# Optimization experiments

Hardware: AMD Instinct MI355X
Metric: run time of the kernel (lower is better)

## Reference

```python
import jax, jax.numpy as jnp
import numpy as np

QMIN, QMAX = -128.0, 127.0  # 8-bit signed activation range


def fq_act(x, s):
    """Fake-quantize activations: clip(round(x/s))*s with straight-through estimator."""
    y = jnp.clip(jnp.round(x / s), QMIN, QMAX) * s
    return x + jax.lax.stop_gradient(y - x)


def fq_weight(w):
    """Per-tensor max-abs symmetric (narrow-range) 8-bit weight fake-quant with STE."""
    s = jnp.max(jnp.abs(w)) / 127.0
    y = jnp.clip(jnp.round(w / s), -127.0, 127.0) * s
    return w + jax.lax.stop_gradient(y - w)


def conv1x1(x, w, b):
    # x: [b,c,h,w], w: [o,c] -> [b,o,h,w]
    return jnp.einsum('bchw,oc->bohw', x, w) + b[None, :, None, None]


def setup_inputs() -> dict:
    key = jax.random.key(0)
    ks = jax.random.split(key, 6)
    B, C, HC, H, W = 8, 64, 32, 64, 64
    x = jax.random.normal(ks[0], (B, C, H, W), dtype=jnp.float32)
    wq = jax.random.normal(ks[1], (HC, C), dtype=jnp.float32) * 0.05
    wk = jax.random.normal(ks[2], (HC, C), dtype=jnp.float32) * 0.05
    wv = jax.random.normal(ks[3], (HC, C), dtype=jnp.float32) * 0.05
    wp = jax.random.normal(ks[4], (C, HC), dtype=jnp.float32) * 0.05
    return {
        'x': x,
        'wq': wq, 'bq': jnp.zeros((HC,), jnp.float32),
        'wk': wk, 'bk': jnp.zeros((HC,), jnp.float32),
        'wv': wv, 'bv': jnp.zeros((HC,), jnp.float32),
        'wp': wp, 'bp': jnp.zeros((C,), jnp.float32),
        's_in': jnp.ones((1,), jnp.float32) * 0.0625,
        's_out': jnp.ones((1,), jnp.float32) * 0.0625,
    }


def reference(x, wq, bq, wk, bk, wv, bv, wp, bp, s_in, s_out):
    b, c, h, w = x.shape
    hc = wq.shape[0]
    n = h * w
    xq = fq_act(x, s_in)                              # quant_inp(x)
    q = conv1x1(xq, fq_weight(wq), bq).reshape(b, hc, n).transpose(0, 2, 1)  # [b,n,hc]
    k = conv1x1(xq, fq_weight(wk), bk).reshape(b, hc, n)                     # [b,hc,n]
    v = conv1x1(xq, fq_weight(wv), bv).reshape(b, hc, n).transpose(0, 2, 1)  # [b,n,hc]
    z = jax.nn.softmax(jnp.einsum('bqc,bck->bqk', q, k), axis=-1)            # [b,n,n]
    z = jnp.einsum('bqk,bkc->bqc', z, v).transpose(0, 2, 1).reshape(b, hc, h, w)
    z = fq_act(z, s_in)                               # quant_inp(z) (shared module/scale)
    out = xq + conv1x1(z, fq_weight(wp), bp)
    return fq_act(out, s_out)                         # self.act QuantIdentity
```

## Files before the change

### kernel.cpp

```cpp
#include <hip/hip_runtime.h>
#include <hip/hip_bf16.h>
#include <cstdint>
#include <cstddef>

#define NB 8
#define NC 64
#define NHC 32
#define NN 4096
#define LOG2E 1.44269504088896340736f

typedef short v8s __attribute__((ext_vector_type(8)));
typedef float v4f __attribute__((ext_vector_type(4)));
typedef unsigned int v4u __attribute__((ext_vector_type(4)));

__device__ __forceinline__ unsigned short f2b(float f) {
    unsigned int u = __builtin_bit_cast(unsigned int, f);
    u += 0x7fffu + ((u >> 16) & 1u);
    return (unsigned short)(u >> 16);
}
__device__ __forceinline__ float b2f(unsigned short s) {
    unsigned int u = ((unsigned int)s) << 16;
    return __builtin_bit_cast(float, u);
}
__device__ __forceinline__ unsigned int pack2_bf16(float a, float b) {
    unsigned int ua = __builtin_bit_cast(unsigned int, a);
    ua += 0x7fffu + ((ua >> 16) & 1u);
    unsigned int ub = __builtin_bit_cast(unsigned int, b);
    ub += 0x7fffu + ((ub >> 16) & 1u);
    return (ua >> 16) | (ub & 0xffff0000u);
}
__device__ __forceinline__ unsigned int trunc2_bf16(float a, float b) {
    return __builtin_amdgcn_perm(__builtin_bit_cast(unsigned int, b),
                                 __builtin_bit_cast(unsigned int, a), 0x07060302u);
}
__device__ __forceinline__ float wave_max(float v) {
    #pragma unroll
    for (int off = 1; off < 64; off <<= 1) v = fmaxf(v, __shfl_xor(v, off));
    return v;
}

__global__ __launch_bounds__(256) void k_qkv(
    const float* __restrict__ x,
    const float* __restrict__ wq, const float* __restrict__ wk, const float* __restrict__ wv,
    const float* __restrict__ bq, const float* __restrict__ bk, const float* __restrict__ bv,
    const float* __restrict__ s_in,
    unsigned short* __restrict__ xqb, unsigned short* __restrict__ qb,
    unsigned short* __restrict__ kb, unsigned short* __restrict__ vb)
{
    int blk = blockIdx.x;
    int b   = blk & 7;
    int seg = blk >> 3;
    int p0  = seg * 64;
    int tid = threadIdx.x;
    int wave = tid >> 6;
    int lane = tid & 63;

    __shared__ __align__(16) unsigned short xt[64][72];
    __shared__ __align__(16) unsigned short wlds[6144];
    __shared__ float red[3][4];

    float4 q0 = *(const float4*)(wq + tid * 8), q1 = *(const float4*)(wq + tid * 8 + 4);
    float4 k0 = *(const float4*)(wk + tid * 8), k1 = *(const float4*)(wk + tid * 8 + 4);
    float4 v0 = *(const float4*)(wv + tid * 8), v1 = *(const float4*)(wv + tid * 8 + 4);
    float mq = fmaxf(fmaxf(fmaxf(fabsf(q0.x), fabsf(q0.y)), fmaxf(fabsf(q0.z), fabsf(q0.w))),
                     fmaxf(fmaxf(fabsf(q1.x), fabsf(q1.y)), fmaxf(fabsf(q1.z), fabsf(q1.w))));
    float mk = fmaxf(fmaxf(fmaxf(fabsf(k0.x), fabsf(k0.y)), fmaxf(fabsf(k0.z), fabsf(k0.w))),
                     fmaxf(fmaxf(fabsf(k1.x), fabsf(k1.y)), fmaxf(fabsf(k1.z), fabsf(k1.w))));
    float mv = fmaxf(fmaxf(fmaxf(fabsf(v0.x), fabsf(v0.y)), fmaxf(fabsf(v0.z), fabsf(v0.w))),
                     fmaxf(fmaxf(fabsf(v1.x), fabsf(v1.y)), fmaxf(fabsf(v1.z), fabsf(v1.w))));
    mq = wave_max(mq); mk = wave_max(mk); mv = wave_max(mv);
    if (lane == 0) { red[0][wave] = mq; red[1][wave] = mk; red[2][wave] = mv; }
    __syncthreads();
    float sq = fmaxf(fmaxf(red[0][0], red[0][1]), fmaxf(red[0][2], red[0][3])) / 127.0f;
    float sk = fmaxf(fmaxf(red[1][0], red[1][1]), fmaxf(red[1][2], red[1][3])) / 127.0f;
    float sw = fmaxf(fmaxf(red[2][0], red[2][1]), fmaxf(red[2][2], red[2][3])) / 127.0f;
    {
        float eq[8] = {q0.x, q0.y, q0.z, q0.w, q1.x, q1.y, q1.z, q1.w};
        float ek[8] = {k0.x, k0.y, k0.z, k0.w, k1.x, k1.y, k1.z, k1.w};
        float ev[8] = {v0.x, v0.y, v0.z, v0.w, v1.x, v1.y, v1.z, v1.w};
        #pragma unroll
        for (int j = 0; j < 8; ++j) {
            wlds[0 * 2048 + tid * 8 + j] = f2b(fminf(fmaxf(rintf(eq[j] / sq), -127.f), 127.f) * sq);
            wlds[1 * 2048 + tid * 8 + j] = f2b(fminf(fmaxf(rintf(ek[j] / sk), -127.f), 127.f) * sk);
            wlds[2 * 2048 + tid * 8 + j] = f2b(fminf(fmaxf(rintf(ev[j] / sw), -127.f), 127.f) * sw);
        }
    }

    float sv = s_in[0];
    float sinv = 1.0f / sv;
    int jj = tid & 15;
    int c0 = tid >> 4;
    #pragma unroll
    for (int it = 0; it < 4; ++it) {
        int c = c0 + it * 16;
        size_t gi = ((size_t)(b * NC + c) << 12) + p0 + jj * 4;
        float4 xv = *(const float4*)(x + gi);
        float r0 = fminf(fmaxf(rintf(xv.x * sinv), -128.f), 127.f) * sv;
        float r1 = fminf(fmaxf(rintf(xv.y * sinv), -128.f), 127.f) * sv;
        float r2 = fminf(fmaxf(rintf(xv.z * sinv), -128.f), 127.f) * sv;
        float r3 = fminf(fmaxf(rintf(xv.w * sinv), -128.f), 127.f) * sv;
        *(uint2*)(xqb + gi) = make_uint2(pack2_bf16(r0, r1), pack2_bf16(r2, r3));
        xt[jj * 4 + 0][c] = f2b(r0);
        xt[jj * 4 + 1][c] = f2b(r1);
        xt[jj * 4 + 2][c] = f2b(r2);
        xt[jj * 4 + 3][c] = f2b(r3);
    }
    __syncthreads();

    int quad = lane >> 4;
    int l15  = lane & 15;

    v8s bf0 = *(const v8s*)(&xt[wave * 16 + l15][0  + quad * 8]);
    v8s bf1 = *(const v8s*)(&xt[wave * 16 + l15][32 + quad * 8]);

    int pos = p0 + wave * 16 + l15;
    size_t posg = (size_t)b * NN + pos;
    int g_v  = wave >> 1;
    int hi_v = wave & 1;
    int qs   = l15 >> 2;
    int rr   = l15 & 3;
    int jv   = hi_v * 4 + rr;
    size_t fb = (size_t)b * NN * NHC + (size_t)seg * 2048;
    const v4f zc = {0.f, 0.f, 0.f, 0.f};

    #pragma unroll
    for (int rb = 0; rb < 6; ++rb) {
        v8s a0 = *(const v8s*)(wlds + (rb * 16 + l15) * 64 + 0  + quad * 8);
        v8s a1 = *(const v8s*)(wlds + (rb * 16 + l15) * 64 + 32 + quad * 8);
        v4f t   = __builtin_amdgcn_mfma_f32_16x16x32_bf16(a0, bf0, zc, 0, 0, 0);
        v4f acc = __builtin_amdgcn_mfma_f32_16x16x32_bf16(a1, bf1, t, 0, 0, 0);

        int R0 = rb * 16 + quad * 4;
        float vals[4];
        #pragma unroll
        for (int r = 0; r < 4; ++r) {
            int R = R0 + r;
            float bias = (R < 32) ? bq[R] : (R < 64) ? bk[R - 32] : bv[R - 64];
            float vv = acc[r] + bias;
            if (R < 32) vv *= LOG2E;
            vals[r] = vv;
        }
        if (R0 < 32) {
            *(unsigned int*)(qb + posg * NHC + R0)     = pack2_bf16(vals[0], vals[1]);
            *(unsigned int*)(qb + posg * NHC + R0 + 2) = pack2_bf16(vals[2], vals[3]);
        } else if (R0 < 64) {
            int chb = R0 - 32;
            size_t sidx = fb + (size_t)wave * 512 + ((chb >> 3) * 16 + l15) * 8 + (chb & 7);
            *(uint2*)(kb + sidx) = make_uint2(pack2_bf16(vals[0], vals[1]),
                                              pack2_bf16(vals[2], vals[3]));
        } else {
            int h = rb - 4;
            #pragma unroll
            for (int r = 0; r < 4; ++r) {
                int lp = quad * 4 + r;
                size_t sidx = fb + (size_t)(2 * h + g_v) * 512 + (qs * 16 + lp) * 8 + jv;
                vb[sidx] = f2b(vals[r]);
            }
        }
    }
}

__global__ __launch_bounds__(256, 2) void k_attn(
    const unsigned short* __restrict__ qb, const unsigned short* __restrict__ kb,
    const unsigned short* __restrict__ vb, const unsigned short* __restrict__ xqb,
    const float* __restrict__ wp, const float* __restrict__ bp,
    const float* __restrict__ s_in, const float* __restrict__ s_out,
    float* __restrict__ out)
{
    int blk  = blockIdx.x;
    int b    = blk & 7;
    int qt   = blk >> 3;
    int qbase = qt * 64;
    int tid  = threadIdx.x;
    int wave = tid >> 6;
    int lane = tid & 63;
    int quad = lane >> 4;
    int l15  = lane & 15;

    __shared__ __align__(16) float zbuf[4][64][36];
    __shared__ float lbuf[4][64];
    __shared__ __align__(16) unsigned short wpq[2048];
    __shared__ float redw[4];

    {
        float4 a0 = *(const float4*)(wp + tid * 8), a1 = *(const float4*)(wp + tid * 8 + 4);
        float mx = fmaxf(fmaxf(fmaxf(fabsf(a0.x), fabsf(a0.y)), fmaxf(fabsf(a0.z), fabsf(a0.w))),
                         fmaxf(fmaxf(fabsf(a1.x), fabsf(a1.y)), fmaxf(fabsf(a1.z), fabsf(a1.w))));
        mx = wave_max(mx);
        if (lane == 0) redw[wave] = mx;
        __syncthreads();
        float scale = fmaxf(fmaxf(redw[0], redw[1]), fmaxf(redw[2], redw[3])) / 127.0f;
        float e[8] = {a0.x, a0.y, a0.z, a0.w, a1.x, a1.y, a1.z, a1.w};
        #pragma unroll
        for (int j = 0; j < 8; ++j) {
            float r = fminf(fmaxf(rintf(e[j] / scale), -127.f), 127.f);
            wpq[tid * 8 + j] = f2b(r * scale);
        }
    }

    const unsigned short* qbat = qb + (size_t)b * NN * NHC;
    const unsigned short* kft  = kb + (size_t)b * NN * NHC;
    const unsigned short* vft  = vb + (size_t)b * NN * NHC;

    v8s qf[4];
    #pragma unroll
    for (int s = 0; s < 4; ++s)
        qf[s] = *(const v8s*)(qbat + (qbase + s * 16 + l15) * NHC + quad * 8);

    const v4f zc = {0.f, 0.f, 0.f, 0.f};
    v4f zt[4][2] = {{zc, zc}, {zc, zc}, {zc, zc}, {zc, zc}};
    float psA[4] = {0.f, 0.f, 0.f, 0.f};
    float psB[4] = {0.f, 0.f, 0.f, 0.f};

    int lane8 = lane * 8;
    int t0 = wave * 16;

    const unsigned short* kp = kft + (size_t)t0 * 2048;
    const unsigned short* vp = vft + (size_t)t0 * 2048;
    v8s ck0 = *(const v8s*)(kp + 0 * 512 + lane8);
    v8s ck1 = *(const v8s*)(kp + 1 * 512 + lane8);
    v8s ck2 = *(const v8s*)(kp + 2 * 512 + lane8);
    v8s ck3 = *(const v8s*)(kp + 3 * 512 + lane8);
    v8s cv00 = *(const v8s*)(vp + 0 * 512 + lane8);
    v8s cv01 = *(const v8s*)(vp + 1 * 512 + lane8);
    v8s cv10 = *(const v8s*)(vp + 2 * 512 + lane8);
    v8s cv11 = *(const v8s*)(vp + 3 * 512 + lane8);

    #pragma unroll 1
    for (int i = 0; i < 16; ++i) {
        int ni = wave * 16 + ((i + 1) & 15);
        const unsigned short* kn = kft + (size_t)ni * 2048;
        const unsigned short* vn = vft + (size_t)ni * 2048;
        v8s nk0 = *(const v8s*)(kn + 0 * 512 + lane8);
        v8s nk1 = *(const v8s*)(kn + 1 * 512 + lane8);
        v8s nk2 = *(const v8s*)(kn + 2 * 512 + lane8);
        v8s nk3 = *(const v8s*)(kn + 3 * 512 + lane8);
        v8s nv00 = *(const v8s*)(vn + 0 * 512 + lane8);
        v8s nv01 = *(const v8s*)(vn + 1 * 512 + lane8);
        v8s nv10 = *(const v8s*)(vn + 2 * 512 + lane8);
        v8s nv11 = *(const v8s*)(vn + 3 * 512 + lane8);
        __builtin_amdgcn_sched_barrier(0);

        #pragma unroll
        for (int s = 0; s < 4; ++s) {
            v4f sa[4];
            sa[0] = __builtin_amdgcn_mfma_f32_16x16x32_bf16(ck0, qf[s], zc, 0, 0, 0);
            sa[1] = __builtin_amdgcn_mfma_f32_16x16x32_bf16(ck1, qf[s], zc, 0, 0, 0);
            sa[2] = __builtin_amdgcn_mfma_f32_16x16x32_bf16(ck2, qf[s], zc, 0, 0, 0);
            sa[3] = __builtin_amdgcn_mfma_f32_16x16x32_bf16(ck3, qf[s], zc, 0, 0, 0);

            #pragma unroll
            for (int g = 0; g < 2; ++g) {
                float p00 = __builtin_amdgcn_exp2f(sa[2 * g][0]);
                float p01 = __builtin_amdgcn_exp2f(sa[2 * g][1]);
                float p02 = __builtin_amdgcn_exp2f(sa[2 * g][2]);
                float p03 = __builtin_amdgcn_exp2f(sa[2 * g][3]);
                float p10 = __builtin_amdgcn_exp2f(sa[2 * g + 1][0]);
                float p11 = __builtin_amdgcn_exp2f(sa[2 * g + 1][1]);
                float p12 = __builtin_amdgcn_exp2f(sa[2 * g + 1][2]);
                float p13 = __builtin_amdgcn_exp2f(sa[2 * g + 1][3]);
                psA[s] += p00 + p01;
                psB[s] += p02 + p03;
                psA[s] += p10 + p11;
                psB[s] += p12 + p13;
                v4u w;
                w.x = trunc2_bf16(p00, p01);
                w.y = trunc2_bf16(p02, p03);
                w.z = trunc2_bf16(p10, p11);
                w.w = trunc2_bf16(p12, p13);
                v8s pfrag = __builtin_bit_cast(v8s, w);
                if (g == 0) {
                    zt[s][0] = __builtin_amdgcn_mfma_f32_16x16x32_bf16(cv00, pfrag, zt[s][0], 0, 0, 0);
                    zt[s][1] = __builtin_amdgcn_mfma_f32_16x16x32_bf16(cv10, pfrag, zt[s][1], 0, 0, 0);
                } else {
                    zt[s][0] = __builtin_amdgcn_mfma_f32_16x16x32_bf16(cv01, pfrag, zt[s][0], 0, 0, 0);
                    zt[s][1] = __builtin_amdgcn_mfma_f32_16x16x32_bf16(cv11, pfrag, zt[s][1], 0, 0, 0);
                }
            }
        }
        ck0 = nk0; ck1 = nk1; ck2 = nk2; ck3 = nk3;
        cv00 = nv00; cv01 = nv01; cv10 = nv10; cv11 = nv11;
    }

    #pragma unroll
    for (int s = 0; s < 4; ++s) {
        *(v4f*)(&zbuf[wave][s * 16 + l15][     quad * 4]) = zt[s][0];
        *(v4f*)(&zbuf[wave][s * 16 + l15][16 + quad * 4]) = zt[s][1];
        float ps = psA[s] + psB[s];
        ps += __shfl_xor(ps, 16);
        ps += __shfl_xor(ps, 32);
        if (quad == 0) lbuf[wave][s * 16 + l15] = ps;
    }
    __syncthreads();

    int myq = wave * 16 + l15;
    float L = lbuf[0][myq] + lbuf[1][myq] + lbuf[2][myq] + lbuf[3][myq];

    float z[8] = {0.f};
    #pragma unroll
    for (int w = 0; w < 4; ++w) {
        v4f za  = *(const v4f*)(&zbuf[w][myq][quad * 8]);
        v4f zb2 = *(const v4f*)(&zbuf[w][myq][quad * 8 + 4]);
        #pragma unroll
        for (int j = 0; j < 4; ++j) { z[j] += za[j]; z[4 + j] += zb2[j]; }
    }
    float sv = s_in[0], sinv = 1.0f / sv;
    float so = s_out[0], soinv = 1.0f / so;
    float Linv = 1.0f / L;
    unsigned int zp[4];
    #pragma unroll
    for (int jp = 0; jp < 4; ++jp) {
        float a = z[2 * jp]     * Linv;
        float c = z[2 * jp + 1] * Linv;
        a = fminf(fmaxf(rintf(a * sinv), -128.f), 127.f) * sv;
        c = fminf(fmaxf(rintf(c * sinv), -128.f), 127.f) * sv;
        zp[jp] = pack2_bf16(a, c);
    }
    v8s zf = __builtin_bit_cast(v8s, *(uint4*)zp);

    v8s w0f = *(const v8s*)(wpq + ( 0 + l15) * NHC + quad * 8);
    v8s w1f = *(const v8s*)(wpq + (16 + l15) * NHC + quad * 8);
    v8s w2f = *(const v8s*)(wpq + (32 + l15) * NHC + quad * 8);
    v8s w3f = *(const v8s*)(wpq + (48 + l15) * NHC + quad * 8);
    v4f o0 = __builtin_amdgcn_mfma_f32_16x16x32_bf16(w0f, zf, zc, 0, 0, 0);
    v4f o1 = __builtin_amdgcn_mfma_f32_16x16x32_bf16(w1f, zf, zc, 0, 0, 0);
    v4f o2 = __builtin_amdgcn_mfma_f32_16x16x32_bf16(w2f, zf, zc, 0, 0, 0);
    v4f o3 = __builtin_amdgcn_mfma_f32_16x16x32_bf16(w3f, zf, zc, 0, 0, 0);

    int pos = qbase + wave * 16 + l15;
    #pragma unroll
    for (int ot = 0; ot < 4; ++ot) {
        v4f ov = (ot == 0) ? o0 : (ot == 1) ? o1 : (ot == 2) ? o2 : o3;
        #pragma unroll
        for (int r = 0; r < 4; ++r) {
            int oc = ot * 16 + quad * 4 + r;
            size_t idx = (size_t)(b * NC + oc) * NN + pos;
            float val = ov[r] + bp[oc] + b2f(xqb[idx]);
            float f = fminf(fmaxf(rintf(val * soinv), -128.f), 127.f);
            out[idx] = f * so;
        }
    }
}

extern "C" void kernel_launch(void* const* d_in, const int* in_sizes, int n_in,
                              void* d_out, int out_size, void* d_ws, size_t ws_size,
                              hipStream_t stream) {
    const float* x     = (const float*)d_in[0];
    const float* wq    = (const float*)d_in[1];
    const float* bq    = (const float*)d_in[2];
    const float* wk    = (const float*)d_in[3];
    const float* bk    = (const float*)d_in[4];
    const float* wv    = (const float*)d_in[5];
    const float* bv    = (const float*)d_in[6];
    const float* wp    = (const float*)d_in[7];
    const float* bp    = (const float*)d_in[8];
    const float* s_in  = (const float*)d_in[9];
    const float* s_out = (const float*)d_in[10];
    float* out = (float*)d_out;

    char* ws = (char*)d_ws;
    size_t off = 0;
    auto carve = [&](size_t bytes) {
        void* p = ws + off;
        off = (off + bytes + 255) & ~(size_t)255;
        return p;
    };
    unsigned short* xqb = (unsigned short*)carve((size_t)NB * NC * NN * 2);
    unsigned short* qbf = (unsigned short*)carve((size_t)NB * NN * NHC * 2);
    unsigned short* kbf = (unsigned short*)carve((size_t)NB * NN * NHC * 2);
    unsigned short* vbf = (unsigned short*)carve((size_t)NB * NHC * NN * 2);

    hipLaunchKernelGGL(k_qkv, dim3(512), dim3(256), 0, stream,
                       x, wq, wk, wv, bq, bk, bv, s_in, xqb, qbf, kbf, vbf);
    hipLaunchKernelGGL(k_attn, dim3(512), dim3(256), 0, stream,
                       qbf, kbf, vbf, xqb, wp, bp, s_in, s_out, out);
}
```

Measured before the change: 113.2 us.

## Double block size to 512 threads and split query tiles across wave pairs

```diff
diff --git a/kernel.cpp b/kernel.cpp
--- a/kernel.cpp
+++ b/kernel.cpp
@@ -38,8 +38,15 @@
     for (int off = 1; off < 64; off <<= 1) v = fmaxf(v, __shfl_xor(v, off));
     return v;
 }
-
-__global__ __launch_bounds__(256) void k_qkv(
+__device__ __forceinline__ float fmax4a(float4 a) {
+    return fmaxf(fmaxf(fabsf(a.x), fabsf(a.y)), fmaxf(fabsf(a.z), fabsf(a.w)));
+}
+__device__ __forceinline__ float max8(const float* r) {
+    return fmaxf(fmaxf(fmaxf(r[0], r[1]), fmaxf(r[2], r[3])),
+                 fmaxf(fmaxf(r[4], r[5]), fmaxf(r[6], r[7])));
+}
+
+__global__ __launch_bounds__(512) void k_qkv(
     const float* __restrict__ x,
     const float* __restrict__ wq, const float* __restrict__ wk, const float* __restrict__ wv,
     const float* __restrict__ bq, const float* __restrict__ bk, const float* __restrict__ bv,
@@ -57,32 +64,28 @@
 
     __shared__ __align__(16) unsigned short xt[64][72];
     __shared__ __align__(16) unsigned short wlds[6144];
-    __shared__ float red[3][4];
-
-    float4 q0 = *(const float4*)(wq + tid * 8), q1 = *(const float4*)(wq + tid * 8 + 4);
-    float4 k0 = *(const float4*)(wk + tid * 8), k1 = *(const float4*)(wk + tid * 8 + 4);
-    float4 v0 = *(const float4*)(wv + tid * 8), v1 = *(const float4*)(wv + tid * 8 + 4);
-    float mq = fmaxf(fmaxf(fmaxf(fabsf(q0.x), fabsf(q0.y)), fmaxf(fabsf(q0.z), fabsf(q0.w))),
-                     fmaxf(fmaxf(fabsf(q1.x), fabsf(q1.y)), fmaxf(fabsf(q1.z), fabsf(q1.w))));
-    float mk = fmaxf(fmaxf(fmaxf(fabsf(k0.x), fabsf(k0.y)), fmaxf(fabsf(k0.z), fabsf(k0.w))),
-                     fmaxf(fmaxf(fabsf(k1.x), fabsf(k1.y)), fmaxf(fabsf(k1.z), fabsf(k1.w))));
-    float mv = fmaxf(fmaxf(fmaxf(fabsf(v0.x), fabsf(v0.y)), fmaxf(fabsf(v0.z), fabsf(v0.w))),
-                     fmaxf(fmaxf(fabsf(v1.x), fabsf(v1.y)), fmaxf(fabsf(v1.z), fabsf(v1.w))));
-    mq = wave_max(mq); mk = wave_max(mk); mv = wave_max(mv);
+    __shared__ float red[3][8];
+
+    float4 q0 = *(const float4*)(wq + tid * 4);
+    float4 k0 = *(const float4*)(wk + tid * 4);
+    float4 v0 = *(const float4*)(wv + tid * 4);
+    float mq = wave_max(fmax4a(q0));
+    float mk = wave_max(fmax4a(k0));
+    float mv = wave_max(fmax4a(v0));
     if (lane == 0) { red[0][wave] = mq; red[1][wave] = mk; red[2][wave] = mv; }
     __syncthreads();
-    float sq = fmaxf(fmaxf(red[0][0], red[0][1]), fmaxf(red[0][2], red[0][3])) / 127.0f;
-    float sk = fmaxf(fmaxf(red[1][0], red[1][1]), fmaxf(red[1][2], red[1][3])) / 127.0f;
-    float sw = fmaxf(fmaxf(red[2][0], red[2][1]), fmaxf(red[2][2], red[2][3])) / 127.0f;
+    float sq = max8(red[0]) / 127.0f;
+    float sk = max8(red[1]) / 127.0f;
+    float sw = max8(red[2]) / 127.0f;
     {
-        float eq[8] = {q0.x, q0.y, q0.z, q0.w, q1.x, q1.y, q1.z, q1.w};
-        float ek[8] = {k0.x, k0.y, k0.z, k0.w, k1.x, k1.y, k1.z, k1.w};
-        float ev[8] = {v0.x, v0.y, v0.z, v0.w, v1.x, v1.y, v1.z, v1.w};
-        #pragma unroll
-        for (int j = 0; j < 8; ++j) {
-            wlds[0 * 2048 + tid * 8 + j] = f2b(fminf(fmaxf(rintf(eq[j] / sq), -127.f), 127.f) * sq);
-            wlds[1 * 2048 + tid * 8 + j] = f2b(fminf(fmaxf(rintf(ek[j] / sk), -127.f), 127.f) * sk);
-            wlds[2 * 2048 + tid * 8 + j] = f2b(fminf(fmaxf(rintf(ev[j] / sw), -127.f), 127.f) * sw);
+        float eq[4] = {q0.x, q0.y, q0.z, q0.w};
+        float ek[4] = {k0.x, k0.y, k0.z, k0.w};
+        float ev[4] = {v0.x, v0.y, v0.z, v0.w};
+        #pragma unroll
+        for (int j = 0; j < 4; ++j) {
+            wlds[0 * 2048 + tid * 4 + j] = f2b(fminf(fmaxf(rintf(eq[j] / sq), -127.f), 127.f) * sq);
+            wlds[1 * 2048 + tid * 4 + j] = f2b(fminf(fmaxf(rintf(ek[j] / sk), -127.f), 127.f) * sk);
+            wlds[2 * 2048 + tid * 4 + j] = f2b(fminf(fmaxf(rintf(ev[j] / sw), -127.f), 127.f) * sw);
         }
     }
 
@@ -91,8 +94,8 @@
     int jj = tid & 15;
     int c0 = tid >> 4;
     #pragma unroll
-    for (int it = 0; it < 4; ++it) {
-        int c = c0 + it * 16;
+    for (int it = 0; it < 2; ++it) {
+        int c = c0 + it * 32;
         size_t gi = ((size_t)(b * NC + c) << 12) + p0 + jj * 4;
         float4 xv = *(const float4*)(x + gi);
         float r0 = fminf(fmaxf(rintf(xv.x * sinv), -128.f), 127.f) * sv;
@@ -109,14 +112,16 @@
 
     int quad = lane >> 4;
     int l15  = lane & 15;
-
-    v8s bf0 = *(const v8s*)(&xt[wave * 16 + l15][0  + quad * 8]);
-    v8s bf1 = *(const v8s*)(&xt[wave * 16 + l15][32 + quad * 8]);
-
-    int pos = p0 + wave * 16 + l15;
+    int ps   = wave & 3;
+    int rh   = wave >> 2;
+
+    v8s bf0 = *(const v8s*)(&xt[ps * 16 + l15][0  + quad * 8]);
+    v8s bf1 = *(const v8s*)(&xt[ps * 16 + l15][32 + quad * 8]);
+
+    int pos = p0 + ps * 16 + l15;
     size_t posg = (size_t)b * NN + pos;
-    int g_v  = wave >> 1;
-    int hi_v = wave & 1;
+    int g_v  = ps >> 1;
+    int hi_v = ps & 1;
     int qs   = l15 >> 2;
     int rr   = l15 & 3;
     int jv   = hi_v * 4 + rr;
@@ -124,7 +129,8 @@
     const v4f zc = {0.f, 0.f, 0.f, 0.f};
 
     #pragma unroll
-    for (int rb = 0; rb < 6; ++rb) {
+    for (int j = 0; j < 3; ++j) {
+        int rb = rh * 3 + j;
         v8s a0 = *(const v8s*)(wlds + (rb * 16 + l15) * 64 + 0  + quad * 8);
         v8s a1 = *(const v8s*)(wlds + (rb * 16 + l15) * 64 + 32 + quad * 8);
         v4f t   = __builtin_amdgcn_mfma_f32_16x16x32_bf16(a0, bf0, zc, 0, 0, 0);
@@ -145,7 +151,7 @@
             *(unsigned int*)(qb + posg * NHC + R0 + 2) = pack2_bf16(vals[2], vals[3]);
         } else if (R0 < 64) {
             int chb = R0 - 32;
-            size_t sidx = fb + (size_t)wave * 512 + ((chb >> 3) * 16 + l15) * 8 + (chb & 7);
+            size_t sidx = fb + (size_t)ps * 512 + ((chb >> 3) * 16 + l15) * 8 + (chb & 7);
             *(uint2*)(kb + sidx) = make_uint2(pack2_bf16(vals[0], vals[1]),
                                               pack2_bf16(vals[2], vals[3]));
         } else {
@@ -160,7 +166,7 @@
     }
 }
 
-__global__ __launch_bounds__(256, 2) void k_attn(
+__global__ __launch_bounds__(512, 4) void k_attn(
     const unsigned short* __restrict__ qb, const unsigned short* __restrict__ kb,
     const unsigned short* __restrict__ vb, const unsigned short* __restrict__ xqb,
     const float* __restrict__ wp, const float* __restrict__ bp,
@@ -176,25 +182,25 @@
     int lane = tid & 63;
     int quad = lane >> 4;
     int l15  = lane & 15;
+    int wq2  = wave >> 2;
+    int wk4  = wave & 3;
 
     __shared__ __align__(16) float zbuf[4][64][36];
     __shared__ float lbuf[4][64];
     __shared__ __align__(16) unsigned short wpq[2048];
-    __shared__ float redw[4];
+    __shared__ float redw[8];
 
     {
-        float4 a0 = *(const float4*)(wp + tid * 8), a1 = *(const float4*)(wp + tid * 8 + 4);
-        float mx = fmaxf(fmaxf(fmaxf(fabsf(a0.x), fabsf(a0.y)), fmaxf(fabsf(a0.z), fabsf(a0.w))),
-                         fmaxf(fmaxf(fabsf(a1.x), fabsf(a1.y)), fmaxf(fabsf(a1.z), fabsf(a1.w))));
-        mx = wave_max(mx);
+        float4 a0 = *(const float4*)(wp + tid * 4);
+        float mx = wave_max(fmax4a(a0));
         if (lane == 0) redw[wave] = mx;
         __syncthreads();
-        float scale = fmaxf(fmaxf(redw[0], redw[1]), fmaxf(redw[2], redw[3])) / 127.0f;
-        float e[8] = {a0.x, a0.y, a0.z, a0.w, a1.x, a1.y, a1.z, a1.w};
-        #pragma unroll
-        for (int j = 0; j < 8; ++j) {
+        float scale = max8(redw) / 127.0f;
+        float e[4] = {a0.x, a0.y, a0.z, a0.w};
+        #pragma unroll
+        for (int j = 0; j < 4; ++j) {
             float r = fminf(fmaxf(rintf(e[j] / scale), -127.f), 127.f);
-            wpq[tid * 8 + j] = f2b(r * scale);
+            wpq[tid * 4 + j] = f2b(r * scale);
         }
     }
 
@@ -202,47 +208,34 @@
     const unsigned short* kft  = kb + (size_t)b * NN * NHC;
     const unsigned short* vft  = vb + (size_t)b * NN * NHC;
 
-    v8s qf[4];
-    #pragma unroll
-    for (int s = 0; s < 4; ++s)
-        qf[s] = *(const v8s*)(qbat + (qbase + s * 16 + l15) * NHC + quad * 8);
+    v8s qf[2];
+    #pragma unroll
+    for (int s = 0; s < 2; ++s)
+        qf[s] = *(const v8s*)(qbat + (qbase + wq2 * 32 + s * 16 + l15) * NHC + quad * 8);
 
     const v4f zc = {0.f, 0.f, 0.f, 0.f};
-    v4f zt[4][2] = {{zc, zc}, {zc, zc}, {zc, zc}, {zc, zc}};
-    float psA[4] = {0.f, 0.f, 0.f, 0.f};
-    float psB[4] = {0.f, 0.f, 0.f, 0.f};
+    v4f zt[2][2] = {{zc, zc}, {zc, zc}};
+    float psA[2] = {0.f, 0.f};
+    float psB[2] = {0.f, 0.f};
 
     int lane8 = lane * 8;
-    int t0 = wave * 16;
-
-    const unsigned short* kp = kft + (size_t)t0 * 2048;
-    const unsigned short* vp = vft + (size_t)t0 * 2048;
-    v8s ck0 = *(const v8s*)(kp + 0 * 512 + lane8);
-    v8s ck1 = *(const v8s*)(kp + 1 * 512 + lane8);
-    v8s ck2 = *(const v8s*)(kp + 2 * 512 + lane8);
-    v8s ck3 = *(const v8s*)(kp + 3 * 512 + lane8);
-    v8s cv00 = *(const v8s*)(vp + 0 * 512 + lane8);
-    v8s cv01 = *(const v8s*)(vp + 1 * 512 + lane8);
-    v8s cv10 = *(const v8s*)(vp + 2 * 512 + lane8);
-    v8s cv11 = *(const v8s*)(vp + 3 * 512 + lane8);
 
     #pragma unroll 1
     for (int i = 0; i < 16; ++i) {
-        int ni = wave * 16 + ((i + 1) & 15);
-        const unsigned short* kn = kft + (size_t)ni * 2048;
-        const unsigned short* vn = vft + (size_t)ni * 2048;
-        v8s nk0 = *(const v8s*)(kn + 0 * 512 + lane8);
-        v8s nk1 = *(const v8s*)(kn + 1 * 512 + lane8);
-        v8s nk2 = *(const v8s*)(kn + 2 * 512 + lane8);
-        v8s nk3 = *(const v8s*)(kn + 3 * 512 + lane8);
-        v8s nv00 = *(const v8s*)(vn + 0 * 512 + lane8);
-        v8s nv01 = *(const v8s*)(vn + 1 * 512 + lane8);
-        v8s nv10 = *(const v8s*)(vn + 2 * 512 + lane8);
-        v8s nv11 = *(const v8s*)(vn + 3 * 512 + lane8);
-        __builtin_amdgcn_sched_barrier(0);
-
-        #pragma unroll
-        for (int s = 0; s < 4; ++s) {
+        int ti = wk4 * 16 + i;
+        const unsigned short* kp = kft + (size_t)ti * 2048;
+        const unsigned short* vp = vft + (size_t)ti * 2048;
+        v8s ck0 = *(const v8s*)(kp + 0 * 512 + lane8);
+        v8s ck1 = *(const v8s*)(kp + 1 * 512 + lane8);
+        v8s ck2 = *(const v8s*)(kp + 2 * 512 + lane8);
+        v8s ck3 = *(const v8s*)(kp + 3 * 512 + lane8);
+        v8s cv00 = *(const v8s*)(vp + 0 * 512 + lane8);
+        v8s cv01 = *(const v8s*)(vp + 1 * 512 + lane8);
+        v8s cv10 = *(const v8s*)(vp + 2 * 512 + lane8);
+        v8s cv11 = *(const v8s*)(vp + 3 * 512 + lane8);
+
+        #pragma unroll
+        for (int s = 0; s < 2; ++s) {
             v4f sa[4];
             sa[0] = __builtin_amdgcn_mfma_f32_16x16x32_bf16(ck0, qf[s], zc, 0, 0, 0);
             sa[1] = __builtin_amdgcn_mfma_f32_16x16x32_bf16(ck1, qf[s], zc, 0, 0, 0);
@@ -278,66 +271,68 @@
                 }
             }
         }
-        ck0 = nk0; ck1 = nk1; ck2 = nk2; ck3 = nk3;
-        cv00 = nv00; cv01 = nv01; cv10 = nv10; cv11 = nv11;
-    }
-
-    #pragma unroll
-    for (int s = 0; s < 4; ++s) {
-        *(v4f*)(&zbuf[wave][s * 16 + l15][     quad * 4]) = zt[s][0];
-        *(v4f*)(&zbuf[wave][s * 16 + l15][16 + quad * 4]) = zt[s][1];
+    }
+
+    #pragma unroll
+    for (int s = 0; s < 2; ++s) {
+        int row = wq2 * 32 + s * 16 + l15;
+        *(v4f*)(&zbuf[wk4][row][     quad * 4]) = zt[s][0];
+        *(v4f*)(&zbuf[wk4][row][16 + quad * 4]) = zt[s][1];
         float ps = psA[s] + psB[s];
         ps += __shfl_xor(ps, 16);
         ps += __shfl_xor(ps, 32);
-        if (quad == 0) lbuf[wave][s * 16 + l15] = ps;
+        if (quad == 0) lbuf[wk4][row] = ps;
     }
     __syncthreads();
 
-    int myq = wave * 16 + l15;
-    float L = lbuf[0][myq] + lbuf[1][myq] + lbuf[2][myq] + lbuf[3][myq];
-
-    float z[8] = {0.f};
-    #pragma unroll
-    for (int w = 0; w < 4; ++w) {
-        v4f za  = *(const v4f*)(&zbuf[w][myq][quad * 8]);
-        v4f zb2 = *(const v4f*)(&zbuf[w][myq][quad * 8 + 4]);
-        #pragma unroll
-        for (int j = 0; j < 4; ++j) { z[j] += za[j]; z[4 + j] += zb2[j]; }
-    }
-    float sv = s_in[0], sinv = 1.0f / sv;
-    float so = s_out[0], soinv = 1.0f / so;
-    float Linv = 1.0f / L;
-    unsigned int zp[4];
-    #pragma unroll
-    for (int jp = 0; jp < 4; ++jp) {
-        float a = z[2 * jp]     * Linv;
-        float c = z[2 * jp + 1] * Linv;
-        a = fminf(fmaxf(rintf(a * sinv), -128.f), 127.f) * sv;
-        c = fminf(fmaxf(rintf(c * sinv), -128.f), 127.f) * sv;
-        zp[jp] = pack2_bf16(a, c);
-    }
-    v8s zf = __builtin_bit_cast(v8s, *(uint4*)zp);
-
-    v8s w0f = *(const v8s*)(wpq + ( 0 + l15) * NHC + quad * 8);
-    v8s w1f = *(const v8s*)(wpq + (16 + l15) * NHC + quad * 8);
-    v8s w2f = *(const v8s*)(wpq + (32 + l15) * NHC + quad * 8);
-    v8s w3f = *(const v8s*)(wpq + (48 + l15) * NHC + quad * 8);
-    v4f o0 = __builtin_amdgcn_mfma_f32_16x16x32_bf16(w0f, zf, zc, 0, 0, 0);
-    v4f o1 = __builtin_amdgcn_mfma_f32_16x16x32_bf16(w1f, zf, zc, 0, 0, 0);
-    v4f o2 = __builtin_amdgcn_mfma_f32_16x16x32_bf16(w2f, zf, zc, 0, 0, 0);
-    v4f o3 = __builtin_amdgcn_mfma_f32_16x16x32_bf16(w3f, zf, zc, 0, 0, 0);
-
-    int pos = qbase + wave * 16 + l15;
-    #pragma unroll
-    for (int ot = 0; ot < 4; ++ot) {
-        v4f ov = (ot == 0) ? o0 : (ot == 1) ? o1 : (ot == 2) ? o2 : o3;
-        #pragma unroll
-        for (int r = 0; r < 4; ++r) {
-            int oc = ot * 16 + quad * 4 + r;
-            size_t idx = (size_t)(b * NC + oc) * NN + pos;
-            float val = ov[r] + bp[oc] + b2f(xqb[idx]);
-            float f = fminf(fmaxf(rintf(val * soinv), -128.f), 127.f);
-            out[idx] = f * so;
+    if (wave < 4) {
+        int myq = wave * 16 + l15;
+        float L = lbuf[0][myq] + lbuf[1][myq] + lbuf[2][myq] + lbuf[3][myq];
+
+        float z[8] = {0.f};
+        #pragma unroll
+        for (int w = 0; w < 4; ++w) {
+            v4f za  = *(const v4f*)(&zbuf[w][myq][quad * 8]);
+            v4f zb2 = *(const v4f*)(&zbuf[w][myq][quad * 8 + 4]);
+            #pragma unroll
+            for (int j = 0; j < 4; ++j) { z[j] += za[j]; z[4 + j] += zb2[j]; }
+        }
+        float sv = s_in[0], sinv = 1.0f / sv;
+        float so = s_out[0], soinv = 1.0f / so;
+        float Linv = 1.0f / L;
+        unsigned int zp[4];
+        #pragma unroll
+        for (int jp = 0; jp < 4; ++jp) {
+            float a = z[2 * jp]     * Linv;
+            float c = z[2 * jp + 1] * Linv;
+            a = fminf(fmaxf(rintf(a * sinv), -128.f), 127.f) * sv;
+            c = fminf(fmaxf(rintf(c * sinv), -128.f), 127.f) * sv;
+            zp[jp] = pack2_bf16(a, c);
+        }
+        v8s zf = __builtin_bit_cast(v8s, *(uint4*)zp);
+
+        v8s w0f = *(const v8s*)(wpq + ( 0 + l15) * NHC + quad * 8);
+        v8s w1f = *(const v8s*)(wpq + (16 + l15) * NHC + quad * 8);
+        v8s w2f = *(const v8s*)(wpq + (32 + l15) * NHC + quad * 8);
+        v8s w3f = *(const v8s*)(wpq + (48 + l15) * NHC + quad * 8);
+        const v4f zc2 = {0.f, 0.f, 0.f, 0.f};
+        v4f o0 = __builtin_amdgcn_mfma_f32_16x16x32_bf16(w0f, zf, zc2, 0, 0, 0);
+        v4f o1 = __builtin_amdgcn_mfma_f32_16x16x32_bf16(w1f, zf, zc2, 0, 0, 0);
+        v4f o2 = __builtin_amdgcn_mfma_f32_16x16x32_bf16(w2f, zf, zc2, 0, 0, 0);
+        v4f o3 = __builtin_amdgcn_mfma_f32_16x16x32_bf16(w3f, zf, zc2, 0, 0, 0);
+
+        int pos = qbase + wave * 16 + l15;
+        #pragma unroll
+        for (int ot = 0; ot < 4; ++ot) {
+            v4f ov = (ot == 0) ? o0 : (ot == 1) ? o1 : (ot == 2) ? o2 : o3;
+            #pragma unroll
+            for (int r = 0; r < 4; ++r) {
+                int oc = ot * 16 + quad * 4 + r;
+                size_t idx = (size_t)(b * NC + oc) * NN + pos;
+                float val = ov[r] + bp[oc] + b2f(xqb[idx]);
+                float f = fminf(fmaxf(rintf(val * soinv), -128.f), 127.f);
+                out[idx] = f * so;
+            }
         }
     }
 }
@@ -370,8 +365,8 @@
     unsigned short* kbf = (unsigned short*)carve((size_t)NB * NN * NHC * 2);
     unsigned short* vbf = (unsigned short*)carve((size_t)NB * NHC * NN * 2);
 
-    hipLaunchKernelGGL(k_qkv, dim3(512), dim3(256), 0, stream,
+    hipLaunchKernelGGL(k_qkv, dim3(512), dim3(512), 0, stream,
                        x, wq, wk, wv, bq, bk, bv, s_in, xqb, qbf, kbf, vbf);
-    hipLaunchKernelGGL(k_attn, dim3(512), dim3(256), 0, stream,
+    hipLaunchKernelGGL(k_attn, dim3(512), dim3(512), 0, stream,
                        qbf, kbf, vbf, xqb, wp, bp, s_in, s_out, out);
 }
```

New measurement: 113.7 us. Within noise of the previous version (+0.5%).

## Split attention by query rows per wave and stage shared K/V tiles in LDS

Applied to the files above, without the earlier changes.

```diff
diff --git a/kernel.cpp b/kernel.cpp
--- a/kernel.cpp
+++ b/kernel.cpp
@@ -177,8 +177,8 @@
     int quad = lane >> 4;
     int l15  = lane & 15;
 
-    __shared__ __align__(16) float zbuf[4][64][36];
-    __shared__ float lbuf[4][64];
+    __shared__ __align__(16) unsigned short kvbuf[2][4096];
+    __shared__ __align__(16) float zsh[4][16][32];
     __shared__ __align__(16) unsigned short wpq[2048];
     __shared__ float redw[4];
 
@@ -202,130 +202,121 @@
     const unsigned short* kft  = kb + (size_t)b * NN * NHC;
     const unsigned short* vft  = vb + (size_t)b * NN * NHC;
 
-    v8s qf[4];
-    #pragma unroll
-    for (int s = 0; s < 4; ++s)
-        qf[s] = *(const v8s*)(qbat + (qbase + s * 16 + l15) * NHC + quad * 8);
+    v8s qf = *(const v8s*)(qbat + (qbase + wave * 16 + l15) * NHC + quad * 8);
 
     const v4f zc = {0.f, 0.f, 0.f, 0.f};
-    v4f zt[4][2] = {{zc, zc}, {zc, zc}, {zc, zc}, {zc, zc}};
-    float psA[4] = {0.f, 0.f, 0.f, 0.f};
-    float psB[4] = {0.f, 0.f, 0.f, 0.f};
-
-    int lane8 = lane * 8;
-    int t0 = wave * 16;
-
-    const unsigned short* kp = kft + (size_t)t0 * 2048;
-    const unsigned short* vp = vft + (size_t)t0 * 2048;
-    v8s ck0 = *(const v8s*)(kp + 0 * 512 + lane8);
-    v8s ck1 = *(const v8s*)(kp + 1 * 512 + lane8);
-    v8s ck2 = *(const v8s*)(kp + 2 * 512 + lane8);
-    v8s ck3 = *(const v8s*)(kp + 3 * 512 + lane8);
-    v8s cv00 = *(const v8s*)(vp + 0 * 512 + lane8);
-    v8s cv01 = *(const v8s*)(vp + 1 * 512 + lane8);
-    v8s cv10 = *(const v8s*)(vp + 2 * 512 + lane8);
-    v8s cv11 = *(const v8s*)(vp + 3 * 512 + lane8);
-
+    v4f zt0 = zc, zt1 = zc;
+    float psA = 0.f, psB = 0.f;
+
+    auto stage = [&](int t, int bi) {
+        #pragma unroll
+        for (int mm = 0; mm < 2; ++mm) {
+            int m = wave * 2 + mm;
+            const unsigned short* src = (m < 4)
+                ? kft + (size_t)t * 2048 + m * 512
+                : vft + (size_t)t * 2048 + (m - 4) * 512;
+            __builtin_amdgcn_global_load_lds((const void*)(src + lane * 8),
+                                             (void*)(&kvbuf[bi][m * 512]), 16, 0, 0);
+        }
+    };
+
+    stage(0, 0);
+    asm volatile("s_waitcnt vmcnt(0)" ::: "memory");
+    __builtin_amdgcn_s_barrier();
+
+    int cur = 0;
     #pragma unroll 1
-    for (int i = 0; i < 16; ++i) {
-        int ni = wave * 16 + ((i + 1) & 15);
-        const unsigned short* kn = kft + (size_t)ni * 2048;
-        const unsigned short* vn = vft + (size_t)ni * 2048;
-        v8s nk0 = *(const v8s*)(kn + 0 * 512 + lane8);
-        v8s nk1 = *(const v8s*)(kn + 1 * 512 + lane8);
-        v8s nk2 = *(const v8s*)(kn + 2 * 512 + lane8);
-        v8s nk3 = *(const v8s*)(kn + 3 * 512 + lane8);
-        v8s nv00 = *(const v8s*)(vn + 0 * 512 + lane8);
-        v8s nv01 = *(const v8s*)(vn + 1 * 512 + lane8);
-        v8s nv10 = *(const v8s*)(vn + 2 * 512 + lane8);
-        v8s nv11 = *(const v8s*)(vn + 3 * 512 + lane8);
-        __builtin_amdgcn_sched_barrier(0);
-
-        #pragma unroll
-        for (int s = 0; s < 4; ++s) {
-            v4f sa[4];
-            sa[0] = __builtin_amdgcn_mfma_f32_16x16x32_bf16(ck0, qf[s], zc, 0, 0, 0);
-            sa[1] = __builtin_amdgcn_mfma_f32_16x16x32_bf16(ck1, qf[s], zc, 0, 0, 0);
-            sa[2] = __builtin_amdgcn_mfma_f32_16x16x32_bf16(ck2, qf[s], zc, 0, 0, 0);
-            sa[3] = __builtin_amdgcn_mfma_f32_16x16x32_bf16(ck3, qf[s], zc, 0, 0, 0);
-
-            #pragma unroll
-            for (int g = 0; g < 2; ++g) {
-                float p00 = __builtin_amdgcn_exp2f(sa[2 * g][0]);
-                float p01 = __builtin_amdgcn_exp2f(sa[2 * g][1]);
-                float p02 = __builtin_amdgcn_exp2f(sa[2 * g][2]);
-                float p03 = __builtin_amdgcn_exp2f(sa[2 * g][3]);
-                float p10 = __builtin_amdgcn_exp2f(sa[2 * g + 1][0]);
-                float p11 = __builtin_amdgcn_exp2f(sa[2 * g + 1][1]);
-                float p12 = __builtin_amdgcn_exp2f(sa[2 * g + 1][2]);
-                float p13 = __builtin_amdgcn_exp2f(sa[2 * g + 1][3]);
-                psA[s] += p00 + p01;
-                psB[s] += p02 + p03;
-                psA[s] += p10 + p11;
-                psB[s] += p12 + p13;
-                v4u w;
-                w.x = trunc2_bf16(p00, p01);
-                w.y = trunc2_bf16(p02, p03);
-                w.z = trunc2_bf16(p10, p11);
-                w.w = trunc2_bf16(p12, p13);
-                v8s pfrag = __builtin_bit_cast(v8s, w);
-                if (g == 0) {
-                    zt[s][0] = __builtin_amdgcn_mfma_f32_16x16x32_bf16(cv00, pfrag, zt[s][0], 0, 0, 0);
-                    zt[s][1] = __builtin_amdgcn_mfma_f32_16x16x32_bf16(cv10, pfrag, zt[s][1], 0, 0, 0);
-                } else {
-                    zt[s][0] = __builtin_amdgcn_mfma_f32_16x16x32_bf16(cv01, pfrag, zt[s][0], 0, 0, 0);
-                    zt[s][1] = __builtin_amdgcn_mfma_f32_16x16x32_bf16(cv11, pfrag, zt[s][1], 0, 0, 0);
-                }
+    for (int t = 0; t < 64; ++t) {
+        if (t < 63) stage(t + 1, cur ^ 1);
+
+        const unsigned short* kb0 = &kvbuf[cur][0];
+        v8s K0  = *(const v8s*)(kb0 + 0 * 512 + lane * 8);
+        v8s K1  = *(const v8s*)(kb0 + 1 * 512 + lane * 8);
+        v8s K2  = *(const v8s*)(kb0 + 2 * 512 + lane * 8);
+        v8s K3  = *(const v8s*)(kb0 + 3 * 512 + lane * 8);
+        v8s Vv0 = *(const v8s*)(kb0 + 4 * 512 + lane * 8);
+        v8s Vv1 = *(const v8s*)(kb0 + 5 * 512 + lane * 8);
+        v8s Vv2 = *(const v8s*)(kb0 + 6 * 512 + lane * 8);
+        v8s Vv3 = *(const v8s*)(kb0 + 7 * 512 + lane * 8);
+
+        v4f sa[4];
+        sa[0] = __builtin_amdgcn_mfma_f32_16x16x32_bf16(K0, qf, zc, 0, 0, 0);
+        sa[1] = __builtin_amdgcn_mfma_f32_16x16x32_bf16(K1, qf, zc, 0, 0, 0);
+        sa[2] = __builtin_amdgcn_mfma_f32_16x16x32_bf16(K2, qf, zc, 0, 0, 0);
+        sa[3] = __builtin_amdgcn_mfma_f32_16x16x32_bf16(K3, qf, zc, 0, 0, 0);
+
+        #pragma unroll
+        for (int g = 0; g < 2; ++g) {
+            float p00 = __builtin_amdgcn_exp2f(sa[2 * g][0]);
+            float p01 = __builtin_amdgcn_exp2f(sa[2 * g][1]);
+            float p02 = __builtin_amdgcn_exp2f(sa[2 * g][2]);
+            float p03 = __builtin_amdgcn_exp2f(sa[2 * g][3]);
+            float p10 = __builtin_amdgcn_exp2f(sa[2 * g + 1][0]);
+            float p11 = __builtin_amdgcn_exp2f(sa[2 * g + 1][1]);
+            float p12 = __builtin_amdgcn_exp2f(sa[2 * g + 1][2]);
+            float p13 = __builtin_amdgcn_exp2f(sa[2 * g + 1][3]);
+            psA += p00 + p01;
+            psB += p02 + p03;
+            psA += p10 + p11;
+            psB += p12 + p13;
+            v4u w;
+            w.x = trunc2_bf16(p00, p01);
+            w.y = trunc2_bf16(p02, p03);
+            w.z = trunc2_bf16(p10, p11);
+            w.w = trunc2_bf16(p12, p13);
+            v8s pfrag = __builtin_bit_cast(v8s, w);
+            if (g == 0) {
+                zt0 = __builtin_amdgcn_mfma_f32_16x16x32_bf16(Vv0, pfrag, zt0, 0, 0, 0);
+                zt1 = __builtin_amdgcn_mfma_f32_16x16x32_bf16(Vv2, pfrag, zt1, 0, 0, 0);
+            } else {
+                zt0 = __builtin_amdgcn_mfma_f32_16x16x32_bf16(Vv1, pfrag, zt0, 0, 0, 0);
+                zt1 = __builtin_amdgcn_mfma_f32_16x16x32_bf16(Vv3, pfrag, zt1, 0, 0, 0);
             }
         }
-        ck0 = nk0; ck1 = nk1; ck2 = nk2; ck3 = nk3;
-        cv00 = nv00; cv01 = nv01; cv10 = nv10; cv11 = nv11;
-    }
-
-    #pragma unroll
-    for (int s = 0; s < 4; ++s) {
-        *(v4f*)(&zbuf[wave][s * 16 + l15][     quad * 4]) = zt[s][0];
-        *(v4f*)(&zbuf[wave][s * 16 + l15][16 + quad * 4]) = zt[s][1];
-        float ps = psA[s] + psB[s];
-        ps += __shfl_xor(ps, 16);
-        ps += __shfl_xor(ps, 32);
-        if (quad == 0) lbuf[wave][s * 16 + l15] = ps;
-    }
+
+        asm volatile("s_waitcnt vmcnt(0)" ::: "memory");
+        __builtin_amdgcn_s_barrier();
+        cur ^= 1;
+    }
+
+    float ps = psA + psB;
+    ps += __shfl_xor(ps, 16);
+    ps += __shfl_xor(ps, 32);
+    float Linv = 1.0f / ps;
+
+    *(v4f*)(&zsh[wave][l15][quad * 4])      = zt0;
+    *(v4f*)(&zsh[wave][l15][16 + quad * 4]) = zt1;
     __syncthreads();
 
-    int myq = wave * 16 + l15;
-    float L = lbuf[0][myq] + lbuf[1][myq] + lbuf[2][myq] + lbuf[3][myq];
-
-    float z[8] = {0.f};
-    #pragma unroll
-    for (int w = 0; w < 4; ++w) {
-        v4f za  = *(const v4f*)(&zbuf[w][myq][quad * 8]);
-        v4f zb2 = *(const v4f*)(&zbuf[w][myq][quad * 8 + 4]);
-        #pragma unroll
-        for (int j = 0; j < 4; ++j) { z[j] += za[j]; z[4 + j] += zb2[j]; }
-    }
     float sv = s_in[0], sinv = 1.0f / sv;
     float so = s_out[0], soinv = 1.0f / so;
-    float Linv = 1.0f / L;
+    v4f za  = *(const v4f*)(&zsh[wave][l15][quad * 8]);
+    v4f zb2 = *(const v4f*)(&zsh[wave][l15][quad * 8 + 4]);
     unsigned int zp[4];
     #pragma unroll
-    for (int jp = 0; jp < 4; ++jp) {
-        float a = z[2 * jp]     * Linv;
-        float c = z[2 * jp + 1] * Linv;
+    for (int jp = 0; jp < 2; ++jp) {
+        float a = za[2 * jp]     * Linv;
+        float c = za[2 * jp + 1] * Linv;
         a = fminf(fmaxf(rintf(a * sinv), -128.f), 127.f) * sv;
         c = fminf(fmaxf(rintf(c * sinv), -128.f), 127.f) * sv;
         zp[jp] = pack2_bf16(a, c);
+        float a2 = zb2[2 * jp]     * Linv;
+        float c2 = zb2[2 * jp + 1] * Linv;
+        a2 = fminf(fmaxf(rintf(a2 * sinv), -128.f), 127.f) * sv;
+        c2 = fminf(fmaxf(rintf(c2 * sinv), -128.f), 127.f) * sv;
+        zp[2 + jp] = pack2_bf16(a2, c2);
     }
     v8s zf = __builtin_bit_cast(v8s, *(uint4*)zp);
 
+    const v4f zc2 = {0.f, 0.f, 0.f, 0.f};
     v8s w0f = *(const v8s*)(wpq + ( 0 + l15) * NHC + quad * 8);
     v8s w1f = *(const v8s*)(wpq + (16 + l15) * NHC + quad * 8);
     v8s w2f = *(const v8s*)(wpq + (32 + l15) * NHC + quad * 8);
     v8s w3f = *(const v8s*)(wpq + (48 + l15) * NHC + quad * 8);
-    v4f o0 = __builtin_amdgcn_mfma_f32_16x16x32_bf16(w0f, zf, zc, 0, 0, 0);
-    v4f o1 = __builtin_amdgcn_mfma_f32_16x16x32_bf16(w1f, zf, zc, 0, 0, 0);
-    v4f o2 = __builtin_amdgcn_mfma_f32_16x16x32_bf16(w2f, zf, zc, 0, 0, 0);
-    v4f o3 = __builtin_amdgcn_mfma_f32_16x16x32_bf16(w3f, zf, zc, 0, 0, 0);
+    v4f o0 = __builtin_amdgcn_mfma_f32_16x16x32_bf16(w0f, zf, zc2, 0, 0, 0);
+    v4f o1 = __builtin_amdgcn_mfma_f32_16x16x32_bf16(w1f, zf, zc2, 0, 0, 0);
+    v4f o2 = __builtin_amdgcn_mfma_f32_16x16x32_bf16(w2f, zf, zc2, 0, 0, 0);
+    v4f o3 = __builtin_amdgcn_mfma_f32_16x16x32_bf16(w3f, zf, zc2, 0, 0, 0);
 
     int pos = qbase + wave * 16 + l15;
     #pragma unroll
```

New measurement: 131.8 us. +16.5%, slower.
